# Kernel optimization log

Measured on AMD Instinct MI355X. Metric: run time of the kernel, lower is better.

Reference implementation:

```python
import jax, jax.numpy as jnp
import numpy as np


def setup_inputs() -> dict:
    key = jax.random.key(0)
    ks = jax.random.split(key, 8)
    B, T, U, D, H, V = 4, 128, 64, 512, 640, 1024
    return {
        "source_encodings": jax.random.normal(ks[0], (B, T, D), dtype=jnp.float32),
        "source_lengths": jax.random.randint(ks[1], (B,), 1, T + 1).astype(jnp.int32),
        "target_encodings": jax.random.normal(ks[2], (B, U, D), dtype=jnp.float32),
        "target_lengths": jax.random.randint(ks[3], (B,), 1, U + 1).astype(jnp.int32),
        "W1": jax.random.normal(ks[4], (2 * D, H), dtype=jnp.float32) * (1.0 / np.sqrt(2 * D)),
        "b1": jax.random.normal(ks[5], (H,), dtype=jnp.float32) * 0.01,
        "W2": jax.random.normal(ks[6], (H, V), dtype=jnp.float32) * (1.0 / np.sqrt(H)),
        "b2": jax.random.normal(ks[7], (V,), dtype=jnp.float32) * 0.01,
    }


def reference(source_encodings, source_lengths, target_encodings, target_lengths, W1, b1, W2, b2):
    # CONCAT combination: Linear(concat(s, t)) == s @ W1[:D] + t @ W1[D:] + b1.
    # This avoids materializing the [B,T,U,2D] expand+concat tensor while
    # computing identical math to the original torch module.
    D = source_encodings.shape[-1]
    W1s, W1t = W1[:D], W1[D:]
    ps = jnp.einsum("btd,dh->bth", source_encodings, W1s)   # [B,T,H]
    pt = jnp.einsum("bud,dh->buh", target_encodings, W1t)   # [B,U,H]
    h = jnp.tanh(ps[:, :, None, :] + pt[:, None, :, :] + b1)  # [B,T,U,H]
    logits = jnp.einsum("btuh,hv->btuv", h, W2) + b2          # [B,T,U,V]
    # Module is in eval mode (not self.training) -> log_softmax applied.
    out = jax.nn.log_softmax(logits, axis=-1)
    return (out, source_lengths, target_lengths)
```

## Files before the change

### kernel.cpp

```cpp
#include <hip/hip_runtime.h>
#include <hip/hip_bf16.h>

#define B_ 4
#define T_ 128
#define U_ 64
#define D_ 512
#define H_ 640
#define V_ 1024

typedef float f32x4 __attribute__((ext_vector_type(4)));

union U2L { uint2 u; long long l; };
union U4L2 { uint4 u; long long l[2]; };

__global__ __launch_bounds__(640) void k_prep(
    const float* __restrict__ W2, uint2* __restrict__ w2p8,
    const int* __restrict__ slen, const int* __restrict__ tlen,
    float* __restrict__ out_tail,
    const float* __restrict__ src, const float* __restrict__ tgt,
    const float* __restrict__ W1, const float* __restrict__ b1,
    float* __restrict__ ps, float* __restrict__ pt) {
  __shared__ __align__(16) float lin[D_ * 4];
  int bid = blockIdx.x, tid = threadIdx.x;
  if (bid < 192) {
    bool is_t = bid >= 128;
    const float* in; const float* w; float* outp;
    if (!is_t) {
      int r0 = bid * 4;
      in = src + (size_t)r0 * D_; w = W1; outp = ps + (size_t)r0 * H_;
    } else {
      int r0 = (bid - 128) * 4;
      in = tgt + (size_t)r0 * D_; w = W1 + (size_t)D_ * H_; outp = pt + (size_t)r0 * H_;
    }
    for (int idx = tid; idx < 4 * D_; idx += 640) {
      int r = idx >> 9, k = idx & (D_ - 1);
      lin[k * 4 + r] = in[idx];
    }
    __syncthreads();
    float a0 = 0.f, a1 = 0.f, a2 = 0.f, a3 = 0.f;
    int j = tid;
    for (int k = 0; k < D_; ++k) {
      float wv = w[(size_t)k * H_ + j];
      f32x4 x = *(const f32x4*)&lin[k * 4];
      a0 += x[0] * wv; a1 += x[1] * wv; a2 += x[2] * wv; a3 += x[3] * wv;
    }
    float bb = is_t ? b1[j] : 0.f;
    outp[0 * H_ + j] = a0 + bb;
    outp[1 * H_ + j] = a1 + bb;
    outp[2 * H_ + j] = a2 + bb;
    outp[3 * H_ + j] = a3 + bb;
  } else {
    int kq = bid - 192;
    for (int idx = tid; idx < V_; idx += 640) {
      int wid = idx >> 6, rem = idx & 63, nf = rem >> 4, l16 = rem & 15;
      int col = wid * 64 + l16 * 4 + nf;
      float f[8];
      #pragma unroll
      for (int j = 0; j < 8; ++j) f[j] = W2[(size_t)(kq * 8 + j) * V_ + col];
      int d0 = __builtin_amdgcn_cvt_pk_fp8_f32(f[0], f[1], 0, 0);
      d0 = __builtin_amdgcn_cvt_pk_fp8_f32(f[2], f[3], d0, 1);
      int d1 = __builtin_amdgcn_cvt_pk_fp8_f32(f[4], f[5], 0, 0);
      d1 = __builtin_amdgcn_cvt_pk_fp8_f32(f[6], f[7], d1, 1);
      uint2 c; c.x = (unsigned)d0; c.y = (unsigned)d1;
      w2p8[(size_t)kq * 1024 + wid * 64 + (nf >> 1) * 32 + l16 * 2 + (nf & 1)] = c;
    }
    if (bid == 192 && tid < 8)
      out_tail[tid] = (tid < 4) ? (float)slen[tid] : (float)tlen[tid - 4];
  }
}

__global__ __launch_bounds__(1024, 4) void k_joint(
    const float* __restrict__ ps, const float* __restrict__ pt,
    const uint2* __restrict__ w2p8, const float* __restrict__ b2,
    float* __restrict__ out) {
  __shared__ uint2 ldsA[64 * 81];
  __shared__ float red[16][64][2];
  __shared__ float lzs[64];
  int bid = blockIdx.x;
  int xcd = bid & 7;
  int b = xcd >> 1;
  int t = (bid >> 3) + (xcd & 1) * 64;
  int tid = threadIdx.x;
  int lane = tid & 63, wid = tid >> 6;
  int l16 = lane & 15, lg = lane >> 4;
  const float* psrow = ps + (size_t)(b * T_ + t) * H_;

  {
    int gm = tid >> 4;
    int gk = tid & 15;
    const float* ptrow = pt + (size_t)(b * U_ + gm) * H_;
    uint2* wrow = &ldsA[gm * 81];
    #pragma unroll
    for (int i = 0; i < 5; ++i) {
      int kq = i * 16 + gk;
      const float4* pp = (const float4*)(psrow + kq * 8);
      const float4* qq = (const float4*)(ptrow + kq * 8);
      float4 p0 = pp[0], p1 = pp[1];
      float4 q0 = qq[0], q1 = qq[1];
      float x[8] = {p0.x + q0.x, p0.y + q0.y, p0.z + q0.z, p0.w + q0.w,
                    p1.x + q1.x, p1.y + q1.y, p1.z + q1.z, p1.w + q1.w};
      float h[8];
      #pragma unroll
      for (int j = 0; j < 8; ++j) {
        float e = __expf(2.f * x[j]);
        h[j] = 1.f - 2.f * __builtin_amdgcn_rcpf(e + 1.f);
      }
      int d0 = __builtin_amdgcn_cvt_pk_fp8_f32(h[0], h[1], 0, 0);
      d0 = __builtin_amdgcn_cvt_pk_fp8_f32(h[2], h[3], d0, 1);
      int d1 = __builtin_amdgcn_cvt_pk_fp8_f32(h[4], h[5], 0, 0);
      d1 = __builtin_amdgcn_cvt_pk_fp8_f32(h[6], h[7], d1, 1);
      uint2 c; c.x = (unsigned)d0; c.y = (unsigned)d1;
      wrow[kq] = c;
    }
  }
  __syncthreads();

  f32x4 acc[4][4];
  #pragma unroll
  for (int mf = 0; mf < 4; ++mf)
    #pragma unroll
    for (int nf = 0; nf < 4; ++nf) {
      f32x4 z = {0.f, 0.f, 0.f, 0.f};
      acc[mf][nf] = z;
    }

  {
    const uint2* arow = ldsA + l16 * 81 + lg;
    const uint4* bp = (const uint4*)w2p8 + (size_t)lg * 512 + wid * 32 + l16;
    for (int kq0 = 0; kq0 < 80; kq0 += 4) {
      U2L a[4];
      #pragma unroll
      for (int mf = 0; mf < 4; ++mf)
        a[mf].u = arow[mf * (16 * 81) + kq0];
      U4L2 q0, q1;
      const uint4* bpi = bp + (size_t)kq0 * 512;
      q0.u = bpi[0];
      q1.u = bpi[16];
      long long bbl[4] = {q0.l[0], q0.l[1], q1.l[0], q1.l[1]};
      #pragma unroll
      for (int nf = 0; nf < 4; ++nf)
        #pragma unroll
        for (int mf = 0; mf < 4; ++mf)
          acc[mf][nf] = __builtin_amdgcn_mfma_f32_16x16x32_fp8_fp8(
              a[mf].l, bbl[nf], acc[mf][nf], 0, 0, 0);
    }
  }

  {
    f32x4 b2v = *(const f32x4*)&b2[wid * 64 + l16 * 4];
    #pragma unroll
    for (int mf = 0; mf < 4; ++mf)
      #pragma unroll
      for (int nf = 0; nf < 4; ++nf)
        #pragma unroll
        for (int r = 0; r < 4; ++r)
          acc[mf][nf][r] += b2v[nf];
  }

  #pragma unroll
  for (int mf = 0; mf < 4; ++mf)
    #pragma unroll
    for (int r = 0; r < 4; ++r) {
      float pm = -3.4e38f;
      #pragma unroll
      for (int nf = 0; nf < 4; ++nf) pm = fmaxf(pm, acc[mf][nf][r]);
      pm = fmaxf(pm, __shfl_xor(pm, 1));
      pm = fmaxf(pm, __shfl_xor(pm, 2));
      pm = fmaxf(pm, __shfl_xor(pm, 4));
      pm = fmaxf(pm, __shfl_xor(pm, 8));
      float s = 0.f;
      #pragma unroll
      for (int nf = 0; nf < 4; ++nf) s += __expf(acc[mf][nf][r] - pm);
      s += __shfl_xor(s, 1);
      s += __shfl_xor(s, 2);
      s += __shfl_xor(s, 4);
      s += __shfl_xor(s, 8);
      if (l16 == 0) {
        int row = mf * 16 + lg * 4 + r;
        red[wid][row][0] = pm;
        red[wid][row][1] = s;
      }
    }
  __syncthreads();

  if (tid < 64) {
    float M = -3.4e38f;
    #pragma unroll
    for (int w16 = 0; w16 < 16; ++w16) M = fmaxf(M, red[w16][tid][0]);
    float S = 0.f;
    #pragma unroll
    for (int w16 = 0; w16 < 16; ++w16)
      S += red[w16][tid][1] * __expf(red[w16][tid][0] - M);
    lzs[tid] = M + __logf(S);
  }
  __syncthreads();

  float* outb = out + (size_t)(b * T_ + t) * U_ * V_;
  #pragma unroll
  for (int mf = 0; mf < 4; ++mf)
    #pragma unroll
    for (int r = 0; r < 4; ++r) {
      int row = mf * 16 + lg * 4 + r;
      float lz = lzs[row];
      f32x4 o;
      o[0] = acc[mf][0][r] - lz;
      o[1] = acc[mf][1][r] - lz;
      o[2] = acc[mf][2][r] - lz;
      o[3] = acc[mf][3][r] - lz;
      __builtin_nontemporal_store(
          o, (f32x4*)&outb[(size_t)row * V_ + wid * 64 + l16 * 4]);
    }
}

extern "C" void kernel_launch(void* const* d_in, const int* in_sizes, int n_in,
                              void* d_out, int out_size, void* d_ws, size_t ws_size,
                              hipStream_t stream) {
  const float* src = (const float*)d_in[0];
  const int*   slen = (const int*)d_in[1];
  const float* tgt = (const float*)d_in[2];
  const int*   tlen = (const int*)d_in[3];
  const float* W1 = (const float*)d_in[4];
  const float* b1 = (const float*)d_in[5];
  const float* W2 = (const float*)d_in[6];
  const float* b2 = (const float*)d_in[7];
  float* out = (float*)d_out;

  float* ps   = (float*)d_ws;
  float* pt   = ps + 512 * 640;
  uint2* w2p8 = (uint2*)(pt + 256 * 640);

  k_prep<<<272, 640, 0, stream>>>(W2, w2p8, slen, tlen,
                                  out + (size_t)B_ * T_ * U_ * V_,
                                  src, tgt, W1, b1, ps, pt);
  k_joint<<<512, 1024, 0, stream>>>(ps, pt, w2p8, b2, out);
}
```

Baseline: 98.11 us.

## Process two time steps per joint block and eight rows per prep block

k_joint now loops over two consecutive t values per block, halving the grid to 256 blocks. It hoists the pt row pointer and b2 load out of that loop and software-prefetches the next W2 fp8 fragment into registers during the MFMA loop. k_prep handles eight input rows per block instead of four, so each W1 element read is reused across more rows and fewer blocks are launched. The aim is to amortise per-block setup and hide global latency of W2 loads, at the cost of fewer resident blocks for overlapping the large output store stream.

```diff
diff --git a/kernel.cpp b/kernel.cpp
--- a/kernel.cpp
+++ b/kernel.cpp
@@ -20,37 +20,37 @@
     const float* __restrict__ src, const float* __restrict__ tgt,
     const float* __restrict__ W1, const float* __restrict__ b1,
     float* __restrict__ ps, float* __restrict__ pt) {
-  __shared__ __align__(16) float lin[D_ * 4];
+  __shared__ __align__(16) float lin[D_ * 8];
   int bid = blockIdx.x, tid = threadIdx.x;
-  if (bid < 192) {
-    bool is_t = bid >= 128;
-    const float* in; const float* w; float* outp;
-    if (!is_t) {
-      int r0 = bid * 4;
-      in = src + (size_t)r0 * D_; w = W1; outp = ps + (size_t)r0 * H_;
-    } else {
-      int r0 = (bid - 128) * 4;
-      in = tgt + (size_t)r0 * D_; w = W1 + (size_t)D_ * H_; outp = pt + (size_t)r0 * H_;
-    }
-    for (int idx = tid; idx < 4 * D_; idx += 640) {
+  if (bid < 96) {
+    bool is_t = bid >= 64;
+    int r0 = (is_t ? (bid - 64) : bid) * 8;
+    const float* in = (is_t ? tgt : src) + (size_t)r0 * D_;
+    const float* w = is_t ? (W1 + (size_t)D_ * H_) : W1;
+    float* outp = (is_t ? pt : ps) + (size_t)r0 * H_;
+    for (int idx = tid; idx < 8 * D_; idx += 640) {
       int r = idx >> 9, k = idx & (D_ - 1);
-      lin[k * 4 + r] = in[idx];
-    }
-    __syncthreads();
-    float a0 = 0.f, a1 = 0.f, a2 = 0.f, a3 = 0.f;
+      lin[k * 8 + r] = in[idx];
+    }
+    __syncthreads();
+    float a[8];
+    #pragma unroll
+    for (int r = 0; r < 8; ++r) a[r] = 0.f;
     int j = tid;
     for (int k = 0; k < D_; ++k) {
       float wv = w[(size_t)k * H_ + j];
-      f32x4 x = *(const f32x4*)&lin[k * 4];
-      a0 += x[0] * wv; a1 += x[1] * wv; a2 += x[2] * wv; a3 += x[3] * wv;
+      f32x4 x0 = *(const f32x4*)&lin[k * 8];
+      f32x4 x1 = *(const f32x4*)&lin[k * 8 + 4];
+      a[0] += x0[0] * wv; a[1] += x0[1] * wv;
+      a[2] += x0[2] * wv; a[3] += x0[3] * wv;
+      a[4] += x1[0] * wv; a[5] += x1[1] * wv;
+      a[6] += x1[2] * wv; a[7] += x1[3] * wv;
     }
     float bb = is_t ? b1[j] : 0.f;
-    outp[0 * H_ + j] = a0 + bb;
-    outp[1 * H_ + j] = a1 + bb;
-    outp[2 * H_ + j] = a2 + bb;
-    outp[3 * H_ + j] = a3 + bb;
+    #pragma unroll
+    for (int r = 0; r < 8; ++r) outp[(size_t)r * H_ + j] = a[r] + bb;
   } else {
-    int kq = bid - 192;
+    int kq = bid - 96;
     for (int idx = tid; idx < V_; idx += 640) {
       int wid = idx >> 6, rem = idx & 63, nf = rem >> 4, l16 = rem & 15;
       int col = wid * 64 + l16 * 4 + nf;
@@ -64,7 +64,7 @@
       uint2 c; c.x = (unsigned)d0; c.y = (unsigned)d1;
       w2p8[(size_t)kq * 1024 + wid * 64 + (nf >> 1) * 32 + l16 * 2 + (nf & 1)] = c;
     }
-    if (bid == 192 && tid < 8)
+    if (bid == 96 && tid < 8)
       out_tail[tid] = (tid < 4) ? (float)slen[tid] : (float)tlen[tid - 4];
   }
 }
@@ -79,75 +79,81 @@
   int bid = blockIdx.x;
   int xcd = bid & 7;
   int b = xcd >> 1;
-  int t = (bid >> 3) + (xcd & 1) * 64;
+  int t0 = ((bid >> 3) + (xcd & 1) * 32) * 2;
   int tid = threadIdx.x;
   int lane = tid & 63, wid = tid >> 6;
   int l16 = lane & 15, lg = lane >> 4;
-  const float* psrow = ps + (size_t)(b * T_ + t) * H_;
-
-  {
-    int gm = tid >> 4;
-    int gk = tid & 15;
-    const float* ptrow = pt + (size_t)(b * U_ + gm) * H_;
-    uint2* wrow = &ldsA[gm * 81];
-    #pragma unroll
-    for (int i = 0; i < 5; ++i) {
-      int kq = i * 16 + gk;
-      const float4* pp = (const float4*)(psrow + kq * 8);
-      const float4* qq = (const float4*)(ptrow + kq * 8);
-      float4 p0 = pp[0], p1 = pp[1];
-      float4 q0 = qq[0], q1 = qq[1];
-      float x[8] = {p0.x + q0.x, p0.y + q0.y, p0.z + q0.z, p0.w + q0.w,
-                    p1.x + q1.x, p1.y + q1.y, p1.z + q1.z, p1.w + q1.w};
-      float h[8];
-      #pragma unroll
-      for (int j = 0; j < 8; ++j) {
-        float e = __expf(2.f * x[j]);
-        h[j] = 1.f - 2.f * __builtin_amdgcn_rcpf(e + 1.f);
-      }
-      int d0 = __builtin_amdgcn_cvt_pk_fp8_f32(h[0], h[1], 0, 0);
-      d0 = __builtin_amdgcn_cvt_pk_fp8_f32(h[2], h[3], d0, 1);
-      int d1 = __builtin_amdgcn_cvt_pk_fp8_f32(h[4], h[5], 0, 0);
-      d1 = __builtin_amdgcn_cvt_pk_fp8_f32(h[6], h[7], d1, 1);
-      uint2 c; c.x = (unsigned)d0; c.y = (unsigned)d1;
-      wrow[kq] = c;
-    }
-  }
-  __syncthreads();
-
-  f32x4 acc[4][4];
-  #pragma unroll
-  for (int mf = 0; mf < 4; ++mf)
-    #pragma unroll
-    for (int nf = 0; nf < 4; ++nf) {
-      f32x4 z = {0.f, 0.f, 0.f, 0.f};
-      acc[mf][nf] = z;
-    }
-
-  {
-    const uint2* arow = ldsA + l16 * 81 + lg;
-    const uint4* bp = (const uint4*)w2p8 + (size_t)lg * 512 + wid * 32 + l16;
-    for (int kq0 = 0; kq0 < 80; kq0 += 4) {
-      U2L a[4];
-      #pragma unroll
-      for (int mf = 0; mf < 4; ++mf)
-        a[mf].u = arow[mf * (16 * 81) + kq0];
-      U4L2 q0, q1;
-      const uint4* bpi = bp + (size_t)kq0 * 512;
-      q0.u = bpi[0];
-      q1.u = bpi[16];
-      long long bbl[4] = {q0.l[0], q0.l[1], q1.l[0], q1.l[1]};
-      #pragma unroll
-      for (int nf = 0; nf < 4; ++nf)
+  int gm = tid >> 4, gk = tid & 15;
+  const float* ptrow = pt + (size_t)(b * U_ + gm) * H_;
+  f32x4 b2v = *(const f32x4*)&b2[wid * 64 + l16 * 4];
+  const uint2* arow = ldsA + l16 * 81 + lg;
+  const uint4* bp = (const uint4*)w2p8 + (size_t)lg * 512 + wid * 32 + l16;
+
+  for (int ti = 0; ti < 2; ++ti) {
+    int t = t0 + ti;
+    const float* psrow = ps + (size_t)(b * T_ + t) * H_;
+
+    {
+      uint2* wrow = &ldsA[gm * 81];
+      #pragma unroll
+      for (int i = 0; i < 5; ++i) {
+        int kq = i * 16 + gk;
+        const float4* pp = (const float4*)(psrow + kq * 8);
+        const float4* qq = (const float4*)(ptrow + kq * 8);
+        float4 p0 = pp[0], p1 = pp[1];
+        float4 q0 = qq[0], q1 = qq[1];
+        float x[8] = {p0.x + q0.x, p0.y + q0.y, p0.z + q0.z, p0.w + q0.w,
+                      p1.x + q1.x, p1.y + q1.y, p1.z + q1.z, p1.w + q1.w};
+        float h[8];
+        #pragma unroll
+        for (int j = 0; j < 8; ++j) {
+          float e = __expf(2.f * x[j]);
+          h[j] = 1.f - 2.f * __builtin_amdgcn_rcpf(e + 1.f);
+        }
+        int d0 = __builtin_amdgcn_cvt_pk_fp8_f32(h[0], h[1], 0, 0);
+        d0 = __builtin_amdgcn_cvt_pk_fp8_f32(h[2], h[3], d0, 1);
+        int d1 = __builtin_amdgcn_cvt_pk_fp8_f32(h[4], h[5], 0, 0);
+        d1 = __builtin_amdgcn_cvt_pk_fp8_f32(h[6], h[7], d1, 1);
+        uint2 c; c.x = (unsigned)d0; c.y = (unsigned)d1;
+        wrow[kq] = c;
+      }
+    }
+    __syncthreads();
+
+    f32x4 acc[4][4];
+    #pragma unroll
+    for (int mf = 0; mf < 4; ++mf)
+      #pragma unroll
+      for (int nf = 0; nf < 4; ++nf) {
+        f32x4 z = {0.f, 0.f, 0.f, 0.f};
+        acc[mf][nf] = z;
+      }
+
+    {
+      U4L2 q0n, q1n;
+      q0n.u = bp[0];
+      q1n.u = bp[16];
+      for (int kq0 = 0; kq0 < 80; kq0 += 4) {
+        U4L2 q0 = q0n, q1 = q1n;
+        if (kq0 < 76) {
+          const uint4* bpn = bp + (size_t)(kq0 + 4) * 512;
+          q0n.u = bpn[0];
+          q1n.u = bpn[16];
+        }
+        U2L a[4];
         #pragma unroll
         for (int mf = 0; mf < 4; ++mf)
-          acc[mf][nf] = __builtin_amdgcn_mfma_f32_16x16x32_fp8_fp8(
-              a[mf].l, bbl[nf], acc[mf][nf], 0, 0, 0);
-    }
-  }
-
-  {
-    f32x4 b2v = *(const f32x4*)&b2[wid * 64 + l16 * 4];
+          a[mf].u = arow[mf * (16 * 81) + kq0];
+        long long bbl[4] = {q0.l[0], q0.l[1], q1.l[0], q1.l[1]};
+        #pragma unroll
+        for (int nf = 0; nf < 4; ++nf)
+          #pragma unroll
+          for (int mf = 0; mf < 4; ++mf)
+            acc[mf][nf] = __builtin_amdgcn_mfma_f32_16x16x32_fp8_fp8(
+                a[mf].l, bbl[nf], acc[mf][nf], 0, 0, 0);
+      }
+    }
+
     #pragma unroll
     for (int mf = 0; mf < 4; ++mf)
       #pragma unroll
@@ -155,61 +161,61 @@
         #pragma unroll
         for (int r = 0; r < 4; ++r)
           acc[mf][nf][r] += b2v[nf];
+
+    #pragma unroll
+    for (int mf = 0; mf < 4; ++mf)
+      #pragma unroll
+      for (int r = 0; r < 4; ++r) {
+        float pm = -3.4e38f;
+        #pragma unroll
+        for (int nf = 0; nf < 4; ++nf) pm = fmaxf(pm, acc[mf][nf][r]);
+        pm = fmaxf(pm, __shfl_xor(pm, 1));
+        pm = fmaxf(pm, __shfl_xor(pm, 2));
+        pm = fmaxf(pm, __shfl_xor(pm, 4));
+        pm = fmaxf(pm, __shfl_xor(pm, 8));
+        float s = 0.f;
+        #pragma unroll
+        for (int nf = 0; nf < 4; ++nf) s += __expf(acc[mf][nf][r] - pm);
+        s += __shfl_xor(s, 1);
+        s += __shfl_xor(s, 2);
+        s += __shfl_xor(s, 4);
+        s += __shfl_xor(s, 8);
+        if (l16 == 0) {
+          int row = mf * 16 + lg * 4 + r;
+          red[wid][row][0] = pm;
+          red[wid][row][1] = s;
+        }
+      }
+    __syncthreads();
+
+    if (tid < 64) {
+      float M = -3.4e38f;
+      #pragma unroll
+      for (int w16 = 0; w16 < 16; ++w16) M = fmaxf(M, red[w16][tid][0]);
+      float S = 0.f;
+      #pragma unroll
+      for (int w16 = 0; w16 < 16; ++w16)
+        S += red[w16][tid][1] * __expf(red[w16][tid][0] - M);
+      lzs[tid] = M + __logf(S);
+    }
+    __syncthreads();
+
+    float* outb = out + (size_t)(b * T_ + t) * U_ * V_;
+    #pragma unroll
+    for (int mf = 0; mf < 4; ++mf)
+      #pragma unroll
+      for (int r = 0; r < 4; ++r) {
+        int row = mf * 16 + lg * 4 + r;
+        float lz = lzs[row];
+        f32x4 o;
+        o[0] = acc[mf][0][r] - lz;
+        o[1] = acc[mf][1][r] - lz;
+        o[2] = acc[mf][2][r] - lz;
+        o[3] = acc[mf][3][r] - lz;
+        __builtin_nontemporal_store(
+            o, (f32x4*)&outb[(size_t)row * V_ + wid * 64 + l16 * 4]);
+      }
   }
-
-  #pragma unroll
-  for (int mf = 0; mf < 4; ++mf)
-    #pragma unroll
-    for (int r = 0; r < 4; ++r) {
-      float pm = -3.4e38f;
-      #pragma unroll
-      for (int nf = 0; nf < 4; ++nf) pm = fmaxf(pm, acc[mf][nf][r]);
-      pm = fmaxf(pm, __shfl_xor(pm, 1));
-      pm = fmaxf(pm, __shfl_xor(pm, 2));
-      pm = fmaxf(pm, __shfl_xor(pm, 4));
-      pm = fmaxf(pm, __shfl_xor(pm, 8));
-      float s = 0.f;
-      #pragma unroll
-      for (int nf = 0; nf < 4; ++nf) s += __expf(acc[mf][nf][r] - pm);
-      s += __shfl_xor(s, 1);
-      s += __shfl_xor(s, 2);
-      s += __shfl_xor(s, 4);
-      s += __shfl_xor(s, 8);
-      if (l16 == 0) {
-        int row = mf * 16 + lg * 4 + r;
-        red[wid][row][0] = pm;
-        red[wid][row][1] = s;
-      }
-    }
-  __syncthreads();
-
-  if (tid < 64) {
-    float M = -3.4e38f;
-    #pragma unroll
-    for (int w16 = 0; w16 < 16; ++w16) M = fmaxf(M, red[w16][tid][0]);
-    float S = 0.f;
-    #pragma unroll
-    for (int w16 = 0; w16 < 16; ++w16)
-      S += red[w16][tid][1] * __expf(red[w16][tid][0] - M);
-    lzs[tid] = M + __logf(S);
-  }
-  __syncthreads();
-
-  float* outb = out + (size_t)(b * T_ + t) * U_ * V_;
-  #pragma unroll
-  for (int mf = 0; mf < 4; ++mf)
-    #pragma unroll
-    for (int r = 0; r < 4; ++r) {
-      int row = mf * 16 + lg * 4 + r;
-      float lz = lzs[row];
-      f32x4 o;
-      o[0] = acc[mf][0][r] - lz;
-      o[1] = acc[mf][1][r] - lz;
-      o[2] = acc[mf][2][r] - lz;
-      o[3] = acc[mf][3][r] - lz;
-      __builtin_nontemporal_store(
-          o, (f32x4*)&outb[(size_t)row * V_ + wid * 64 + l16 * 4]);
-    }
 }
 
 extern "C" void kernel_launch(void* const* d_in, const int* in_sizes, int n_in,
@@ -229,8 +235,8 @@
   float* pt   = ps + 512 * 640;
   uint2* w2p8 = (uint2*)(pt + 256 * 640);
 
-  k_prep<<<272, 640, 0, stream>>>(W2, w2p8, slen, tlen,
+  k_prep<<<176, 640, 0, stream>>>(W2, w2p8, slen, tlen,
                                   out + (size_t)B_ * T_ * U_ * V_,
                                   src, tgt, W1, b1, ps, pt);
-  k_joint<<<512, 1024, 0, stream>>>(ps, pt, w2p8, b2, out);
+  k_joint<<<256, 1024, 0, stream>>>(ps, pt, w2p8, b2, out);
 }
```

Result: slower. 232.7 us (+137.2%).
